# Kernel optimization log

Measured on AMD Instinct MI355X. Metric: run time of the kernel, lower is better.

The kernel has to match this reference:

```python
import jax, jax.numpy as jnp
import numpy as np

N_ITER = 10
TOL = 1e-05
EPS_R = 1e-10
REG = 1e-06
F32_EPS = float(np.finfo(np.float32).eps)


def setup_inputs() -> dict:
    key = jax.random.key(0)
    K, T, F, _ = 6, 2048, 513, 2
    X = jax.random.normal(key, (K, T, F, 2), dtype=jnp.float32)
    return {"X": X}


def _aux_iva_iss(X):
    # X: (K, T, F, 2) real/imag -> complex (F, K, T)
    Xc = (X[..., 0] + 1j * X[..., 1]).astype(jnp.complex64)
    Xc = jnp.transpose(Xc, (2, 0, 1))  # (F, K, T)
    F, K, T = Xc.shape
    eyeK = jnp.eye(K, dtype=jnp.complex64)
    W = jnp.broadcast_to(eyeK, (F, K, K)).astype(jnp.complex64)  # (F, K, K)
    Xh = jnp.conj(Xc)
    done = jnp.array(False)

    for _ in range(N_ITER):
        W_old = W
        # demix: Y[f] = W[f] @ X[f]
        Y = jnp.einsum('fkm,fmt->fkt', W, Xc)
        # per-(source, frame) norms across frequency
        r = jnp.sqrt(jnp.clip(jnp.sum(jnp.abs(Y) ** 2, axis=0), EPS_R))  # (K, T)
        wt = 1.0 / jnp.clip(r, EPS_R)  # laplace contrast g'(r)/r
        # weighted covariances V[f,k] = (X_f * wt[k]) X_f^H / T + reg*I  -> (F, K, K, K)
        V = jnp.einsum('fat,kt,fbt->fkab', Xc, wt.astype(jnp.complex64), Xh) / T
        V = V + REG * eyeK
        # sequential ISS updates over target row k (vectorized over f, m)
        for k in range(K):
            wk = W[:, k, :]  # (F, K)
            wk_c = jnp.conj(wk)
            quad = jnp.einsum('fa,fmab,fb->fm', wk, V, wk_c)  # w_k V_m w_k^H
            denom = jnp.clip(quad.real, EPS_R)  # (F, K)
            num = jnp.einsum('fma,fmab,fb->fm', W, V, wk_c)  # w_m V_m w_k^H
            vk = num / denom  # (F, K)
            vk = vk.at[:, k].set((1.0 - 1.0 / jnp.sqrt(denom[:, k])).astype(jnp.complex64))
            W = W - vk[:, :, None] * wk[:, None, :]
        # emulate early-break on relative change (freeze W once converged)
        W = jnp.where(done, W_old, W)
        diff = jnp.linalg.norm((W - W_old).reshape(-1))
        rel = diff / jnp.clip(jnp.linalg.norm(W_old.reshape(-1)), F32_EPS)
        done = jnp.logical_or(done, rel < TOL)

    Y = jnp.einsum('fkm,fmt->fkt', W, Xc)  # (F, K, T)
    # ref_mic == 0 -> no projection-back rescaling
    Y_out = jnp.transpose(Y, (1, 2, 0))  # (K, T, F)
    return jnp.stack([Y_out.real, Y_out.imag], axis=-1)  # (K, T, F, 2)


def reference(X):
    return _aux_iva_iss(X)
```

## Files before the change

### kernel.cpp

```cpp
#include <hip/hip_runtime.h>
#include <hip/hip_bf16.h>
#include <math.h>

#define T_DIM 2048
#define F_DIM 513
#define N_ITER 10

#define OFF_W    0
#define OFF_WT   36936
#define OFF_P0   49224
#define OFF_P1   50250
#define OFF_R2   51276
#define OFF_VP   51276

typedef __attribute__((ext_vector_type(8))) short bf16x8;
typedef __attribute__((ext_vector_type(4))) float f32x4;

static __device__ inline unsigned pack2bf(float a, float b) {
    union { __hip_bfloat16 h; unsigned short u; } ca, cb;
    ca.h = __float2bfloat16(a);
    cb.h = __float2bfloat16(b);
    return (unsigned)ca.u | ((unsigned)cb.u << 16);
}

__global__ __launch_bounds__(256) void transp(const float2* __restrict__ X,
                                              float2* __restrict__ Xt,
                                              float* __restrict__ ws) {
    const int fb  = blockIdx.x + 64 * (blockIdx.y + 17 * blockIdx.z);
    const int tid = threadIdx.x;
    if (fb < 73) {
        int idx = fb * 256 + tid;
        if (idx < F_DIM * 36) {
            int e = idx % 36;
            ws[OFF_W + 2 * idx]     = ((e / 6) == (e % 6)) ? 1.0f : 0.0f;
            ws[OFF_W + 2 * idx + 1] = 0.0f;
        }
    } else if (fb < 78) {
        int idx = (fb - 73) * 256 + tid;
        if (idx < 2 * F_DIM) { ws[OFF_P0 + idx] = 1.0f; ws[OFF_P1 + idx] = 1.0f; }
    }

    __shared__ float2 tile[32][33];
    const int k  = blockIdx.z;
    const int t0 = blockIdx.x * 32;
    const int f0 = blockIdx.y * 32;
    const int tx = tid & 31, ty = tid >> 5;
#pragma unroll
    for (int j = 0; j < 4; ++j) {
        int t = t0 + ty + j * 8;
        int f = f0 + tx;
        if (f < F_DIM) tile[ty + j * 8][tx] = X[((size_t)k * T_DIM + t) * F_DIM + f];
    }
    __syncthreads();
#pragma unroll
    for (int j = 0; j < 4; ++j) {
        int f = f0 + ty + j * 8;
        int t = t0 + tx;
        if (f < F_DIM) Xt[((size_t)f * 6 + k) * T_DIM + t] = tile[tx][ty + j * 8];
    }
}

__global__ __launch_bounds__(256) void passA1(const float2* __restrict__ Xt,
                                              float* __restrict__ ws,
                                              const float* __restrict__ pin) {
    __shared__ float r2s[4][6][65];
    __shared__ float sc[8];
    const int tid = threadIdx.x, wv = tid >> 6, lane = tid & 63;
    {
        float d2 = 0.f, o2 = 0.f;
        for (int i = tid; i < F_DIM; i += 256) { d2 += pin[2 * i]; o2 += pin[2 * i + 1]; }
#pragma unroll
        for (int d = 1; d < 64; d <<= 1) { d2 += __shfl_xor(d2, d); o2 += __shfl_xor(o2, d); }
        if (lane == 0) { sc[wv * 2] = d2; sc[wv * 2 + 1] = o2; }
        __syncthreads();
        d2 = sc[0] + sc[2] + sc[4] + sc[6];
        o2 = sc[1] + sc[3] + sc[5] + sc[7];
        float rel = sqrtf(d2) / fmaxf(sqrtf(o2), 1.1920929e-07f);
        if (rel < 1e-5f) return;
    }
    const int t  = blockIdx.x * 64 + lane;
    const int fc = blockIdx.y;
    const float2* Wc = (const float2*)(ws + OFF_W);
    float acc[6] = {0.f, 0.f, 0.f, 0.f, 0.f, 0.f};
#pragma unroll
    for (int i = 0; i < 4; ++i) {
        const int f = fc * 16 + wv * 4 + i;
        if (f < F_DIM) {
            const float2* xf = Xt + (size_t)f * 6 * T_DIM + t;
            float2 x[6];
#pragma unroll
            for (int m = 0; m < 6; ++m) x[m] = xf[(size_t)m * T_DIM];
            const float2* wf = Wc + f * 36;
#pragma unroll
            for (int k = 0; k < 6; ++k) {
                float yr = 0.f, yi = 0.f;
#pragma unroll
                for (int m = 0; m < 6; ++m) {
                    float2 wk = wf[k * 6 + m];
                    yr += wk.x * x[m].x - wk.y * x[m].y;
                    yi += wk.x * x[m].y + wk.y * x[m].x;
                }
                acc[k] += yr * yr + yi * yi;
            }
        }
    }
#pragma unroll
    for (int k = 0; k < 6; ++k) r2s[wv][k][lane] = acc[k];
    __syncthreads();
    for (int v = tid; v < 384; v += 256) {
        int k = v >> 6, l = v & 63;
        float s = r2s[0][k][l] + r2s[1][k][l] + r2s[2][k][l] + r2s[3][k][l];
        ws[OFF_R2 + ((size_t)fc * 6 + k) * T_DIM + blockIdx.x * 64 + l] = s;
    }
}

__global__ __launch_bounds__(256) void passA2(float* __restrict__ ws,
                                              const float* __restrict__ pin) {
    __shared__ float sc[8];
    const int tid = threadIdx.x, wv = tid >> 6, lane = tid & 63;
    {
        float d2 = 0.f, o2 = 0.f;
        for (int i = tid; i < F_DIM; i += 256) { d2 += pin[2 * i]; o2 += pin[2 * i + 1]; }
#pragma unroll
        for (int d = 1; d < 64; d <<= 1) { d2 += __shfl_xor(d2, d); o2 += __shfl_xor(o2, d); }
        if (lane == 0) { sc[wv * 2] = d2; sc[wv * 2 + 1] = o2; }
        __syncthreads();
        d2 = sc[0] + sc[2] + sc[4] + sc[6];
        o2 = sc[1] + sc[3] + sc[5] + sc[7];
        float rel = sqrtf(d2) / fmaxf(sqrtf(o2), 1.1920929e-07f);
        if (rel < 1e-5f) return;
    }
    const int idx = blockIdx.x * 256 + tid;
    float s = 0.f;
#pragma unroll
    for (int fc = 0; fc < 33; ++fc) s += ws[OFF_R2 + (size_t)fc * 6 * T_DIM + idx];
    float r = sqrtf(fmaxf(s, 1e-10f));
    ws[OFF_WT + idx] = 1.0f / fmaxf(r, 1e-10f);
}

__global__ __launch_bounds__(384) void passB(const float2* __restrict__ Xt,
                                             float* __restrict__ ws,
                                             const float* __restrict__ pin) {
    __shared__ __align__(16) char plane[16 * 528];
    __shared__ __align__(16) float gbuf[6][256];
    __shared__ float sc[12];
    const int tid = threadIdx.x, wv = tid >> 6, lane = tid & 63;

    {
        float d2 = 0.f, o2 = 0.f;
        for (int i = tid; i < F_DIM; i += 384) { d2 += pin[2 * i]; o2 += pin[2 * i + 1]; }
#pragma unroll
        for (int d = 1; d < 64; d <<= 1) { d2 += __shfl_xor(d2, d); o2 += __shfl_xor(o2, d); }
        if (lane == 0) { sc[wv * 2] = d2; sc[wv * 2 + 1] = o2; }
        __syncthreads();
        d2 = 0.f; o2 = 0.f;
#pragma unroll
        for (int w = 0; w < 6; ++w) { d2 += sc[w * 2]; o2 += sc[w * 2 + 1]; }
        float rel = sqrtf(d2) / fmaxf(sqrtf(o2), 1.1920929e-07f);
        __syncthreads();
        if (rel < 1e-5f) return;
    }

    const int f = blockIdx.x, tq = blockIdx.y;
    const float2* xb = Xt + (size_t)f * 6 * T_DIM;

    for (int i = tid; i < 528; i += 384) ((unsigned*)(plane + 12 * 528))[i] = 0;

    f32x4 acc0 = {0.f, 0.f, 0.f, 0.f};
    f32x4 acc1 = {0.f, 0.f, 0.f, 0.f};
    const int rc = lane & 15;
    const int G  = lane >> 4;
    const char* pu = plane + rc * 528 + G * 16;
    const float* gk = &gbuf[wv][0] + G * 8;

    for (int c = 0; c < 2; ++c) {
        const int t0 = tq * 512 + c * 256;
        __syncthreads();
        for (int i = tid; i < 1536; i += 384) {
            int kk = i >> 8, toff = i & 255;
            gbuf[kk][toff] = ws[OFF_WT + kk * T_DIM + t0 + toff];
        }
        for (int it = tid; it < 768; it += 384) {
            int m = it >> 7, q = it & 127;
            float4 xv = *(const float4*)(xb + (size_t)m * T_DIM + t0 + 2 * q);
            *(unsigned*)(plane + m * 528 + 4 * q)       = pack2bf(xv.x, xv.z);
            *(unsigned*)(plane + (6 + m) * 528 + 4 * q) = pack2bf(xv.y, xv.w);
        }
        __syncthreads();
#pragma unroll
        for (int s = 0; s < 8; ++s) {
            bf16x8 b = *(const bf16x8*)(pu + s * 64);
            f32x4 gA = *(const f32x4*)(gk + s * 32);
            f32x4 gB = *(const f32x4*)(gk + s * 32 + 4);
            const unsigned* bu = (const unsigned*)&b;
            bf16x8 a;
            unsigned* au = (unsigned*)&a;
            au[0] = pack2bf(__uint_as_float(bu[0] << 16) * gA[0],
                            __uint_as_float(bu[0] & 0xffff0000u) * gA[1]);
            au[1] = pack2bf(__uint_as_float(bu[1] << 16) * gA[2],
                            __uint_as_float(bu[1] & 0xffff0000u) * gA[3]);
            au[2] = pack2bf(__uint_as_float(bu[2] << 16) * gB[0],
                            __uint_as_float(bu[2] & 0xffff0000u) * gB[1]);
            au[3] = pack2bf(__uint_as_float(bu[3] << 16) * gB[2],
                            __uint_as_float(bu[3] & 0xffff0000u) * gB[3]);
            if (s & 1) acc1 = __builtin_amdgcn_mfma_f32_16x16x32_bf16(a, b, acc1, 0, 0, 0);
            else       acc0 = __builtin_amdgcn_mfma_f32_16x16x32_bf16(a, b, acc0, 0, 0, 0);
        }
    }
    __syncthreads();

    float* S = (float*)plane;
    {
        float* Sk = S + wv * 256;
#pragma unroll
        for (int r = 0; r < 4; ++r)
            Sk[(4 * G + r) * 16 + rc] = acc0[r] + acc1[r];
    }
    __syncthreads();

    if (tid < 216) {
        const int kk = tid / 36, e = tid % 36;
        const float* Sk = S + kk * 256;
        float val;
        if (e < 6) {
            val = Sk[e * 16 + e] + Sk[(6 + e) * 16 + (6 + e)];
        } else if (e < 21) {
            int p = e - 6;
            int a = (p < 1) ? 1 : (p < 3) ? 2 : (p < 6) ? 3 : (p < 10) ? 4 : 5;
            int b = p - a * (a - 1) / 2;
            val = Sk[a * 16 + b] + Sk[(6 + a) * 16 + (6 + b)];
        } else {
            int p = e - 21;
            int a = (p < 1) ? 1 : (p < 3) ? 2 : (p < 6) ? 3 : (p < 10) ? 4 : 5;
            int b = p - a * (a - 1) / 2;
            val = Sk[(6 + a) * 16 + b] - Sk[a * 16 + (6 + b)];
        }
        ws[OFF_VP + ((size_t)f * 4 + tq) * 216 + tid] = val;
    }
}

__global__ __launch_bounds__(64) void passC(float* __restrict__ ws,
                                            const float* __restrict__ pin,
                                            float* __restrict__ pout) {
    __shared__ float VL[432];
    const int f = blockIdx.x;
    const int lane = threadIdx.x;
    {
        float d2 = 0.f, o2 = 0.f;
        for (int i = lane; i < F_DIM; i += 64) { d2 += pin[2 * i]; o2 += pin[2 * i + 1]; }
#pragma unroll
        for (int d = 1; d < 64; d <<= 1) { d2 += __shfl_xor(d2, d); o2 += __shfl_xor(o2, d); }
        float rel = sqrtf(d2) / fmaxf(sqrtf(o2), 1.1920929e-07f);
        if (rel < 1e-5f) {
            if (lane == 0) { pout[2 * f] = 0.0f; pout[2 * f + 1] = 1.0f; }
            return;
        }
    }
    for (int v = lane; v < 216; v += 64) {
        float sum = 0.f;
#pragma unroll
        for (int tq = 0; tq < 4; ++tq)
            sum += ws[OFF_VP + ((size_t)f * 4 + tq) * 216 + v];
        sum *= (1.0f / (float)T_DIM);
        int kk = v / 36, e = v % 36;
        if (e < 6) {
            VL[((kk * 6 + e) * 6 + e) * 2]     = sum + 1e-6f;
            VL[((kk * 6 + e) * 6 + e) * 2 + 1] = 0.f;
        } else if (e < 21) {
            int p = e - 6;
            int a = (p < 1) ? 1 : (p < 3) ? 2 : (p < 6) ? 3 : (p < 10) ? 4 : 5;
            int b = p - a * (a - 1) / 2;
            VL[((kk * 6 + a) * 6 + b) * 2] = sum;
            VL[((kk * 6 + b) * 6 + a) * 2] = sum;
        } else {
            int p = e - 21;
            int a = (p < 1) ? 1 : (p < 3) ? 2 : (p < 6) ? 3 : (p < 10) ? 4 : 5;
            int b = p - a * (a - 1) / 2;
            VL[((kk * 6 + a) * 6 + b) * 2 + 1] =  sum;
            VL[((kk * 6 + b) * 6 + a) * 2 + 1] = -sum;
        }
    }
    __syncthreads();

    const int m = lane;
    const bool act = (m < 6);
    float w6[6][2], wold[6][2];
#pragma unroll
    for (int a = 0; a < 6; ++a) {
        w6[a][0] = 0.f; w6[a][1] = 0.f; wold[a][0] = 0.f; wold[a][1] = 0.f;
    }
    float* Wp = ws + OFF_W + ((size_t)f * 36 + (act ? m : 0) * 6) * 2;
    if (act) {
#pragma unroll
        for (int a = 0; a < 6; ++a) {
            w6[a][0] = Wp[2 * a]; w6[a][1] = Wp[2 * a + 1];
            wold[a][0] = w6[a][0]; wold[a][1] = w6[a][1];
        }
    }
    const float2* VL2 = (const float2*)VL;
    for (int kk = 0; kk < 6; ++kk) {
        float wk[6][2];
#pragma unroll
        for (int a = 0; a < 6; ++a) {
            wk[a][0] = __shfl(w6[a][0], kk);
            wk[a][1] = __shfl(w6[a][1], kk);
        }
        if (act) {
            float t6[6][2];
#pragma unroll
            for (int a = 0; a < 6; ++a) {
                float tr = 0.f, ti = 0.f;
#pragma unroll
                for (int b = 0; b < 6; ++b) {
                    float2 vv = VL2[m * 36 + a * 6 + b];
                    tr += vv.x * wk[b][0] + vv.y * wk[b][1];
                    ti += vv.y * wk[b][0] - vv.x * wk[b][1];
                }
                t6[a][0] = tr; t6[a][1] = ti;
            }
            float quad = 0.f, nr = 0.f, ni = 0.f;
#pragma unroll
            for (int a = 0; a < 6; ++a) {
                quad += wk[a][0] * t6[a][0] - wk[a][1] * t6[a][1];
                nr   += w6[a][0] * t6[a][0] - w6[a][1] * t6[a][1];
                ni   += w6[a][0] * t6[a][1] + w6[a][1] * t6[a][0];
            }
            float denom = fmaxf(quad, 1e-10f);
            float vkr, vki;
            if (m == kk) { vkr = 1.0f - 1.0f / sqrtf(denom); vki = 0.0f; }
            else { float inv = 1.0f / denom; vkr = nr * inv; vki = ni * inv; }
#pragma unroll
            for (int a = 0; a < 6; ++a) {
                w6[a][0] -= vkr * wk[a][0] - vki * wk[a][1];
                w6[a][1] -= vkr * wk[a][1] + vki * wk[a][0];
            }
        }
    }
    float d2 = 0.f, o2 = 0.f;
    if (act) {
#pragma unroll
        for (int a = 0; a < 6; ++a) {
            Wp[2 * a] = w6[a][0]; Wp[2 * a + 1] = w6[a][1];
            float dr = w6[a][0] - wold[a][0], di = w6[a][1] - wold[a][1];
            d2 += dr * dr + di * di;
            o2 += wold[a][0] * wold[a][0] + wold[a][1] * wold[a][1];
        }
    }
#pragma unroll
    for (int d = 1; d < 8; d <<= 1) {
        d2 += __shfl_xor(d2, d);
        o2 += __shfl_xor(o2, d);
    }
    if (lane == 0) {
        pout[2 * f]     = d2;
        pout[2 * f + 1] = o2;
    }
}

__global__ __launch_bounds__(256) void finalY(const float2* __restrict__ X,
                                              const float* __restrict__ ws,
                                              float2* __restrict__ out) {
    const int f  = blockIdx.y * 256 + threadIdx.x;
    const int t0 = blockIdx.x * 4;
    if (f >= F_DIM) return;
    const float2* Wf = (const float2*)(ws + OFF_W) + (size_t)f * 36;
    float2 w[36];
#pragma unroll
    for (int i = 0; i < 36; ++i) w[i] = Wf[i];
#pragma unroll
    for (int tl = 0; tl < 4; ++tl) {
        int t = t0 + tl;
        float2 x[6];
#pragma unroll
        for (int m = 0; m < 6; ++m) x[m] = X[((size_t)m * T_DIM + t) * F_DIM + f];
#pragma unroll
        for (int k = 0; k < 6; ++k) {
            float yr = 0.f, yi = 0.f;
#pragma unroll
            for (int m = 0; m < 6; ++m) {
                float2 wk = w[k * 6 + m];
                yr += wk.x * x[m].x - wk.y * x[m].y;
                yi += wk.x * x[m].y + wk.y * x[m].x;
            }
            out[((size_t)k * T_DIM + t) * F_DIM + f] = make_float2(yr, yi);
        }
    }
}

extern "C" void kernel_launch(void* const* d_in, const int* in_sizes, int n_in,
                              void* d_out, int out_size, void* d_ws, size_t ws_size,
                              hipStream_t stream) {
    (void)in_sizes; (void)n_in; (void)out_size; (void)ws_size;
    const float2* X = (const float2*)d_in[0];
    float* ws = (float*)d_ws;
    float2* out = (float2*)d_out;
    float2* Xt = out;

    transp<<<dim3(64, 17, 6), 256, 0, stream>>>(X, Xt, ws);
    for (int it = 0; it < N_ITER; ++it) {
        const float* pin = ws + (((it + 1) & 1) ? OFF_P1 : OFF_P0);
        float* pout      = ws + (((it    ) & 1) ? OFF_P1 : OFF_P0);
        passA1<<<dim3(32, 33), 256, 0, stream>>>(Xt, ws, pin);
        passA2<<<48, 256, 0, stream>>>(ws, pin);
        passB<<<dim3(F_DIM, 4), 384, 0, stream>>>(Xt, ws, pin);
        passC<<<F_DIM, 64, 0, stream>>>(ws, pin, pout);
    }
    finalY<<<dim3(T_DIM / 4, 3), 256, 0, stream>>>(X, ws, out);
}
```

Measured before the change: 620.1 us.

## Fuse ISS update into demix pass, atomically accumulate norms, fold weights into passB

Merges the previous iteration's ISS row update (old passC) into the start of the demix/norm kernel, so each block recomputes W for its 16 frequencies redundantly across time tiles. W is double-buffered to avoid read/write races. Per-frequency-chunk partial norms are combined with atomicAdd into ping-pong accumulators instead of a separate reduction kernel, and passB computes the inverse-norm weights on the fly and zeroes the next accumulator. This cuts launches per iteration from four to two, at the cost of redundant ISS compute and atomic traffic.

New measurement: 594.9 us. 4.1% less time.

```diff
diff --git a/kernel.cpp b/kernel.cpp
--- a/kernel.cpp
+++ b/kernel.cpp
@@ -6,12 +6,13 @@
 #define F_DIM 513
 #define N_ITER 10
 
-#define OFF_W    0
-#define OFF_WT   36936
-#define OFF_P0   49224
-#define OFF_P1   50250
-#define OFF_R2   51276
-#define OFF_VP   51276
+#define OFF_W0   0
+#define OFF_W1   36936
+#define OFF_P0   73872
+#define OFF_P1   74898
+#define OFF_RA0  75924
+#define OFF_RA1  88212
+#define OFF_VP   100500
 
 typedef __attribute__((ext_vector_type(8))) short bf16x8;
 typedef __attribute__((ext_vector_type(4))) float f32x4;
@@ -21,6 +22,25 @@
     ca.h = __float2bfloat16(a);
     cb.h = __float2bfloat16(b);
     return (unsigned)ca.u | ((unsigned)cb.u << 16);
+}
+
+static __device__ inline void scatterV(float* V6, int e, float sum) {
+    if (e < 6) {
+        V6[(e * 6 + e) * 2]     = sum + 1e-6f;
+        V6[(e * 6 + e) * 2 + 1] = 0.f;
+    } else if (e < 21) {
+        int p = e - 6;
+        int a = (p < 1) ? 1 : (p < 3) ? 2 : (p < 6) ? 3 : (p < 10) ? 4 : 5;
+        int b = p - a * (a - 1) / 2;
+        V6[(a * 6 + b) * 2] = sum;
+        V6[(b * 6 + a) * 2] = sum;
+    } else {
+        int p = e - 21;
+        int a = (p < 1) ? 1 : (p < 3) ? 2 : (p < 6) ? 3 : (p < 10) ? 4 : 5;
+        int b = p - a * (a - 1) / 2;
+        V6[(a * 6 + b) * 2 + 1] =  sum;
+        V6[(b * 6 + a) * 2 + 1] = -sum;
+    }
 }
 
 __global__ __launch_bounds__(256) void transp(const float2* __restrict__ X,
@@ -32,12 +52,15 @@
         int idx = fb * 256 + tid;
         if (idx < F_DIM * 36) {
             int e = idx % 36;
-            ws[OFF_W + 2 * idx]     = ((e / 6) == (e % 6)) ? 1.0f : 0.0f;
-            ws[OFF_W + 2 * idx + 1] = 0.0f;
+            ws[OFF_W0 + 2 * idx]     = ((e / 6) == (e % 6)) ? 1.0f : 0.0f;
+            ws[OFF_W0 + 2 * idx + 1] = 0.0f;
         }
     } else if (fb < 78) {
         int idx = (fb - 73) * 256 + tid;
         if (idx < 2 * F_DIM) { ws[OFF_P0 + idx] = 1.0f; ws[OFF_P1 + idx] = 1.0f; }
+    } else if (fb < 126) {
+        int idx = (fb - 78) * 256 + tid;
+        if (idx < 12288) ws[OFF_RA0 + idx] = 0.0f;
     }
 
     __shared__ float2 tile[32][33];
@@ -60,12 +83,21 @@
     }
 }
 
-__global__ __launch_bounds__(256) void passA1(const float2* __restrict__ Xt,
-                                              float* __restrict__ ws,
-                                              const float* __restrict__ pin) {
-    __shared__ float r2s[4][6][65];
+__global__ __launch_bounds__(256) void passA1C(const float2* __restrict__ Xt,
+                                               float* __restrict__ ws,
+                                               const float* __restrict__ pin,
+                                               float* __restrict__ pout,
+                                               const float* __restrict__ wOld,
+                                               float* __restrict__ wNew,
+                                               float* __restrict__ r2acc,
+                                               int do_iss) {
+    __shared__ float Wl[16][72];
+    __shared__ float VL[16][432];
     __shared__ float sc[8];
     const int tid = threadIdx.x, wv = tid >> 6, lane = tid & 63;
+    const int tc = blockIdx.x, fc = blockIdx.y;
+
+    bool frozen;
     {
         float d2 = 0.f, o2 = 0.f;
         for (int i = tid; i < F_DIM; i += 256) { d2 += pin[2 * i]; o2 += pin[2 * i + 1]; }
@@ -76,75 +108,173 @@
         d2 = sc[0] + sc[2] + sc[4] + sc[6];
         o2 = sc[1] + sc[3] + sc[5] + sc[7];
         float rel = sqrtf(d2) / fmaxf(sqrtf(o2), 1.1920929e-07f);
-        if (rel < 1e-5f) return;
-    }
-    const int t  = blockIdx.x * 64 + lane;
-    const int fc = blockIdx.y;
-    const float2* Wc = (const float2*)(ws + OFF_W);
-    float acc[6] = {0.f, 0.f, 0.f, 0.f, 0.f, 0.f};
+        frozen = (rel < 1e-5f);
+        __syncthreads();
+    }
+
+    const int fl = wv * 4 + (lane >> 4);
+    const int f  = fc * 16 + fl;
+    const int m  = lane & 15;
+    const bool act = (f < F_DIM) && (m < 6);
+
+    if (do_iss == 0) {
+        if (act) {
+            const float* Wp = wOld + ((size_t)f * 36 + m * 6) * 2;
+#pragma unroll
+            for (int a = 0; a < 6; ++a) {
+                Wl[fl][(m * 6 + a) * 2]     = Wp[2 * a];
+                Wl[fl][(m * 6 + a) * 2 + 1] = Wp[2 * a + 1];
+            }
+        }
+    } else if (frozen) {
+        if (act) {
+            const float* Wp = wOld + ((size_t)f * 36 + m * 6) * 2;
+            float* Wq = wNew + ((size_t)f * 36 + m * 6) * 2;
+#pragma unroll
+            for (int a = 0; a < 6; ++a) {
+                float v0 = Wp[2 * a], v1 = Wp[2 * a + 1];
+                Wq[2 * a] = v0; Wq[2 * a + 1] = v1;
+                Wl[fl][(m * 6 + a) * 2] = v0; Wl[fl][(m * 6 + a) * 2 + 1] = v1;
+            }
+        }
+        if (tc == 0 && m == 0 && f < F_DIM) { pout[2 * f] = 0.f; pout[2 * f + 1] = 1.f; }
+    } else {
+        if (f < F_DIM) {
+            const float* vp = ws + OFF_VP + (size_t)f * 4 * 216;
+            for (int v = m; v < 216; v += 16) {
+                float sum = (vp[v] + vp[216 + v] + vp[432 + v] + vp[648 + v]) * (1.0f / (float)T_DIM);
+                scatterV(&VL[fl][(v / 36) * 72], v % 36, sum);
+            }
+        }
+        __syncthreads();
+        float w6[6][2], wo6[6][2];
+#pragma unroll
+        for (int a = 0; a < 6; ++a) { w6[a][0] = 0.f; w6[a][1] = 0.f; wo6[a][0] = 0.f; wo6[a][1] = 0.f; }
+        if (act) {
+            const float* Wp = wOld + ((size_t)f * 36 + m * 6) * 2;
+#pragma unroll
+            for (int a = 0; a < 6; ++a) {
+                w6[a][0] = Wp[2 * a]; w6[a][1] = Wp[2 * a + 1];
+                wo6[a][0] = w6[a][0]; wo6[a][1] = w6[a][1];
+            }
+        }
+        const float2* Vm = (const float2*)&VL[fl][0];
+        for (int kk = 0; kk < 6; ++kk) {
+            float wk[6][2];
+#pragma unroll
+            for (int a = 0; a < 6; ++a) {
+                wk[a][0] = __shfl(w6[a][0], kk, 16);
+                wk[a][1] = __shfl(w6[a][1], kk, 16);
+            }
+            if (act) {
+                float t6[6][2];
+#pragma unroll
+                for (int a = 0; a < 6; ++a) {
+                    float tr = 0.f, ti = 0.f;
+#pragma unroll
+                    for (int b = 0; b < 6; ++b) {
+                        float2 vv = Vm[m * 36 + a * 6 + b];
+                        tr += vv.x * wk[b][0] + vv.y * wk[b][1];
+                        ti += vv.y * wk[b][0] - vv.x * wk[b][1];
+                    }
+                    t6[a][0] = tr; t6[a][1] = ti;
+                }
+                float quad = 0.f, nr = 0.f, ni = 0.f;
+#pragma unroll
+                for (int a = 0; a < 6; ++a) {
+                    quad += wk[a][0] * t6[a][0] - wk[a][1] * t6[a][1];
+                    nr   += w6[a][0] * t6[a][0] - w6[a][1] * t6[a][1];
+                    ni   += w6[a][0] * t6[a][1] + w6[a][1] * t6[a][0];
+                }
+                float denom = fmaxf(quad, 1e-10f);
+                float vkr, vki;
+                if (m == kk) { vkr = 1.0f - 1.0f / sqrtf(denom); vki = 0.0f; }
+                else { float inv = 1.0f / denom; vkr = nr * inv; vki = ni * inv; }
+#pragma unroll
+                for (int a = 0; a < 6; ++a) {
+                    w6[a][0] -= vkr * wk[a][0] - vki * wk[a][1];
+                    w6[a][1] -= vkr * wk[a][1] + vki * wk[a][0];
+                }
+            }
+        }
+        float d2 = 0.f, o2 = 0.f;
+        if (act) {
+            float* Wq = wNew + ((size_t)f * 36 + m * 6) * 2;
+#pragma unroll
+            for (int a = 0; a < 6; ++a) {
+                Wq[2 * a] = w6[a][0]; Wq[2 * a + 1] = w6[a][1];
+                Wl[fl][(m * 6 + a) * 2] = w6[a][0]; Wl[fl][(m * 6 + a) * 2 + 1] = w6[a][1];
+                float dr = w6[a][0] - wo6[a][0], di = w6[a][1] - wo6[a][1];
+                d2 += dr * dr + di * di;
+                o2 += wo6[a][0] * wo6[a][0] + wo6[a][1] * wo6[a][1];
+            }
+        }
+#pragma unroll
+        for (int d = 1; d < 8; d <<= 1) {
+            d2 += __shfl_xor(d2, d);
+            o2 += __shfl_xor(o2, d);
+        }
+        if (tc == 0 && m == 0 && f < F_DIM) { pout[2 * f] = d2; pout[2 * f + 1] = o2; }
+    }
+    __syncthreads();
+    if (do_iss && frozen) return;
+
+    float* r2s = &VL[0][0];
+    const int t2 = tc * 128 + lane * 2;
+    float acc[6][2];
+#pragma unroll
+    for (int k = 0; k < 6; ++k) { acc[k][0] = 0.f; acc[k][1] = 0.f; }
 #pragma unroll
     for (int i = 0; i < 4; ++i) {
-        const int f = fc * 16 + wv * 4 + i;
-        if (f < F_DIM) {
-            const float2* xf = Xt + (size_t)f * 6 * T_DIM + t;
-            float2 x[6];
-#pragma unroll
-            for (int m = 0; m < 6; ++m) x[m] = xf[(size_t)m * T_DIM];
-            const float2* wf = Wc + f * 36;
+        const int ff = fc * 16 + wv * 4 + i;
+        if (ff < F_DIM) {
+            const float2* xf = Xt + (size_t)ff * 6 * T_DIM;
+            float4 x4[6];
+#pragma unroll
+            for (int mm = 0; mm < 6; ++mm)
+                x4[mm] = *(const float4*)(xf + (size_t)mm * T_DIM + t2);
+            const float* wrow = Wl[wv * 4 + i];
 #pragma unroll
             for (int k = 0; k < 6; ++k) {
-                float yr = 0.f, yi = 0.f;
-#pragma unroll
-                for (int m = 0; m < 6; ++m) {
-                    float2 wk = wf[k * 6 + m];
-                    yr += wk.x * x[m].x - wk.y * x[m].y;
-                    yi += wk.x * x[m].y + wk.y * x[m].x;
+                float y0r = 0.f, y0i = 0.f, y1r = 0.f, y1i = 0.f;
+#pragma unroll
+                for (int mm = 0; mm < 6; ++mm) {
+                    float wr = wrow[(k * 6 + mm) * 2], wi = wrow[(k * 6 + mm) * 2 + 1];
+                    y0r += wr * x4[mm].x - wi * x4[mm].y;
+                    y0i += wr * x4[mm].y + wi * x4[mm].x;
+                    y1r += wr * x4[mm].z - wi * x4[mm].w;
+                    y1i += wr * x4[mm].w + wi * x4[mm].z;
                 }
-                acc[k] += yr * yr + yi * yi;
-            }
-        }
-    }
-#pragma unroll
-    for (int k = 0; k < 6; ++k) r2s[wv][k][lane] = acc[k];
-    __syncthreads();
-    for (int v = tid; v < 384; v += 256) {
-        int k = v >> 6, l = v & 63;
-        float s = r2s[0][k][l] + r2s[1][k][l] + r2s[2][k][l] + r2s[3][k][l];
-        ws[OFF_R2 + ((size_t)fc * 6 + k) * T_DIM + blockIdx.x * 64 + l] = s;
-    }
-}
-
-__global__ __launch_bounds__(256) void passA2(float* __restrict__ ws,
-                                              const float* __restrict__ pin) {
-    __shared__ float sc[8];
-    const int tid = threadIdx.x, wv = tid >> 6, lane = tid & 63;
-    {
-        float d2 = 0.f, o2 = 0.f;
-        for (int i = tid; i < F_DIM; i += 256) { d2 += pin[2 * i]; o2 += pin[2 * i + 1]; }
-#pragma unroll
-        for (int d = 1; d < 64; d <<= 1) { d2 += __shfl_xor(d2, d); o2 += __shfl_xor(o2, d); }
-        if (lane == 0) { sc[wv * 2] = d2; sc[wv * 2 + 1] = o2; }
-        __syncthreads();
-        d2 = sc[0] + sc[2] + sc[4] + sc[6];
-        o2 = sc[1] + sc[3] + sc[5] + sc[7];
-        float rel = sqrtf(d2) / fmaxf(sqrtf(o2), 1.1920929e-07f);
-        if (rel < 1e-5f) return;
-    }
-    const int idx = blockIdx.x * 256 + tid;
-    float s = 0.f;
-#pragma unroll
-    for (int fc = 0; fc < 33; ++fc) s += ws[OFF_R2 + (size_t)fc * 6 * T_DIM + idx];
-    float r = sqrtf(fmaxf(s, 1e-10f));
-    ws[OFF_WT + idx] = 1.0f / fmaxf(r, 1e-10f);
+                acc[k][0] += y0r * y0r + y0i * y0i;
+                acc[k][1] += y1r * y1r + y1i * y1i;
+            }
+        }
+    }
+    __syncthreads();
+#pragma unroll
+    for (int k = 0; k < 6; ++k) {
+        r2s[(wv * 6 + k) * 128 + lane * 2]     = acc[k][0];
+        r2s[(wv * 6 + k) * 128 + lane * 2 + 1] = acc[k][1];
+    }
+    __syncthreads();
+    for (int v = tid; v < 768; v += 256) {
+        int k = v >> 7, l = v & 127;
+        float s = r2s[(0 * 6 + k) * 128 + l] + r2s[(1 * 6 + k) * 128 + l]
+                + r2s[(2 * 6 + k) * 128 + l] + r2s[(3 * 6 + k) * 128 + l];
+        atomicAdd(&r2acc[k * T_DIM + tc * 128 + l], s);
+    }
 }
 
 __global__ __launch_bounds__(384) void passB(const float2* __restrict__ Xt,
                                              float* __restrict__ ws,
-                                             const float* __restrict__ pin) {
+                                             const float* __restrict__ pin,
+                                             const float* __restrict__ r2in,
+                                             float* __restrict__ r2zero) {
     __shared__ __align__(16) char plane[16 * 528];
     __shared__ __align__(16) float gbuf[6][256];
     __shared__ float sc[12];
     const int tid = threadIdx.x, wv = tid >> 6, lane = tid & 63;
+    const int f = blockIdx.x, tq = blockIdx.y;
 
     {
         float d2 = 0.f, o2 = 0.f;
@@ -161,7 +291,15 @@
         if (rel < 1e-5f) return;
     }
 
-    const int f = blockIdx.x, tq = blockIdx.y;
+    {
+        int bb = (f * 4 + tq) * 6;
+#pragma unroll
+        for (int i = 0; i < 6; ++i) {
+            int idx = bb + i;
+            if (idx < 12288) r2zero[idx] = 0.f;
+        }
+    }
+
     const float2* xb = Xt + (size_t)f * 6 * T_DIM;
 
     for (int i = tid; i < 528; i += 384) ((unsigned*)(plane + 12 * 528))[i] = 0;
@@ -178,13 +316,15 @@
         __syncthreads();
         for (int i = tid; i < 1536; i += 384) {
             int kk = i >> 8, toff = i & 255;
-            gbuf[kk][toff] = ws[OFF_WT + kk * T_DIM + t0 + toff];
+            float s = r2in[kk * T_DIM + t0 + toff];
+            float r = sqrtf(fmaxf(s, 1e-10f));
+            gbuf[kk][toff] = 1.0f / fmaxf(r, 1e-10f);
         }
         for (int it = tid; it < 768; it += 384) {
-            int m = it >> 7, q = it & 127;
-            float4 xv = *(const float4*)(xb + (size_t)m * T_DIM + t0 + 2 * q);
-            *(unsigned*)(plane + m * 528 + 4 * q)       = pack2bf(xv.x, xv.z);
-            *(unsigned*)(plane + (6 + m) * 528 + 4 * q) = pack2bf(xv.y, xv.w);
+            int mm = it >> 7, q = it & 127;
+            float4 xv = *(const float4*)(xb + (size_t)mm * T_DIM + t0 + 2 * q);
+            *(unsigned*)(plane + mm * 528 + 4 * q)       = pack2bf(xv.x, xv.z);
+            *(unsigned*)(plane + (6 + mm) * 528 + 4 * q) = pack2bf(xv.y, xv.w);
         }
         __syncthreads();
 #pragma unroll
@@ -241,7 +381,9 @@
 
 __global__ __launch_bounds__(64) void passC(float* __restrict__ ws,
                                             const float* __restrict__ pin,
-                                            float* __restrict__ pout) {
+                                            float* __restrict__ pout,
+                                            const float* __restrict__ wOld,
+                                            float* __restrict__ wNew) {
     __shared__ float VL[432];
     const int f = blockIdx.x;
     const int lane = threadIdx.x;
@@ -252,52 +394,35 @@
         for (int d = 1; d < 64; d <<= 1) { d2 += __shfl_xor(d2, d); o2 += __shfl_xor(o2, d); }
         float rel = sqrtf(d2) / fmaxf(sqrtf(o2), 1.1920929e-07f);
         if (rel < 1e-5f) {
+            for (int v = lane; v < 72; v += 64)
+                wNew[(size_t)f * 72 + v] = wOld[(size_t)f * 72 + v];
             if (lane == 0) { pout[2 * f] = 0.0f; pout[2 * f + 1] = 1.0f; }
             return;
         }
     }
-    for (int v = lane; v < 216; v += 64) {
-        float sum = 0.f;
-#pragma unroll
-        for (int tq = 0; tq < 4; ++tq)
-            sum += ws[OFF_VP + ((size_t)f * 4 + tq) * 216 + v];
-        sum *= (1.0f / (float)T_DIM);
-        int kk = v / 36, e = v % 36;
-        if (e < 6) {
-            VL[((kk * 6 + e) * 6 + e) * 2]     = sum + 1e-6f;
-            VL[((kk * 6 + e) * 6 + e) * 2 + 1] = 0.f;
-        } else if (e < 21) {
-            int p = e - 6;
-            int a = (p < 1) ? 1 : (p < 3) ? 2 : (p < 6) ? 3 : (p < 10) ? 4 : 5;
-            int b = p - a * (a - 1) / 2;
-            VL[((kk * 6 + a) * 6 + b) * 2] = sum;
-            VL[((kk * 6 + b) * 6 + a) * 2] = sum;
-        } else {
-            int p = e - 21;
-            int a = (p < 1) ? 1 : (p < 3) ? 2 : (p < 6) ? 3 : (p < 10) ? 4 : 5;
-            int b = p - a * (a - 1) / 2;
-            VL[((kk * 6 + a) * 6 + b) * 2 + 1] =  sum;
-            VL[((kk * 6 + b) * 6 + a) * 2 + 1] = -sum;
+    {
+        const float* vp = ws + OFF_VP + (size_t)f * 4 * 216;
+        for (int v = lane; v < 216; v += 64) {
+            float sum = (vp[v] + vp[216 + v] + vp[432 + v] + vp[648 + v]) * (1.0f / (float)T_DIM);
+            scatterV(&VL[(v / 36) * 72], v % 36, sum);
         }
     }
     __syncthreads();
 
     const int m = lane;
     const bool act = (m < 6);
-    float w6[6][2], wold[6][2];
-#pragma unroll
-    for (int a = 0; a < 6; ++a) {
-        w6[a][0] = 0.f; w6[a][1] = 0.f; wold[a][0] = 0.f; wold[a][1] = 0.f;
-    }
-    float* Wp = ws + OFF_W + ((size_t)f * 36 + (act ? m : 0) * 6) * 2;
+    float w6[6][2], wo6[6][2];
+#pragma unroll
+    for (int a = 0; a < 6; ++a) { w6[a][0] = 0.f; w6[a][1] = 0.f; wo6[a][0] = 0.f; wo6[a][1] = 0.f; }
     if (act) {
+        const float* Wp = wOld + ((size_t)f * 36 + m * 6) * 2;
 #pragma unroll
         for (int a = 0; a < 6; ++a) {
             w6[a][0] = Wp[2 * a]; w6[a][1] = Wp[2 * a + 1];
-            wold[a][0] = w6[a][0]; wold[a][1] = w6[a][1];
-        }
-    }
-    const float2* VL2 = (const float2*)VL;
+            wo6[a][0] = w6[a][0]; wo6[a][1] = w6[a][1];
+        }
+    }
+    const float2* Vm = (const float2*)VL;
     for (int kk = 0; kk < 6; ++kk) {
         float wk[6][2];
 #pragma unroll
@@ -312,7 +437,7 @@
                 float tr = 0.f, ti = 0.f;
 #pragma unroll
                 for (int b = 0; b < 6; ++b) {
-                    float2 vv = VL2[m * 36 + a * 6 + b];
+                    float2 vv = Vm[m * 36 + a * 6 + b];
                     tr += vv.x * wk[b][0] + vv.y * wk[b][1];
                     ti += vv.y * wk[b][0] - vv.x * wk[b][1];
                 }
@@ -338,12 +463,13 @@
     }
     float d2 = 0.f, o2 = 0.f;
     if (act) {
+        float* Wq = wNew + ((size_t)f * 36 + m * 6) * 2;
 #pragma unroll
         for (int a = 0; a < 6; ++a) {
-            Wp[2 * a] = w6[a][0]; Wp[2 * a + 1] = w6[a][1];
-            float dr = w6[a][0] - wold[a][0], di = w6[a][1] - wold[a][1];
+            Wq[2 * a] = w6[a][0]; Wq[2 * a + 1] = w6[a][1];
+            float dr = w6[a][0] - wo6[a][0], di = w6[a][1] - wo6[a][1];
             d2 += dr * dr + di * di;
-            o2 += wold[a][0] * wold[a][0] + wold[a][1] * wold[a][1];
+            o2 += wo6[a][0] * wo6[a][0] + wo6[a][1] * wo6[a][1];
         }
     }
 #pragma unroll
@@ -363,7 +489,7 @@
     const int f  = blockIdx.y * 256 + threadIdx.x;
     const int t0 = blockIdx.x * 4;
     if (f >= F_DIM) return;
-    const float2* Wf = (const float2*)(ws + OFF_W) + (size_t)f * 36;
+    const float2* Wf = (const float2*)(ws + OFF_W0) + (size_t)f * 36;
     float2 w[36];
 #pragma unroll
     for (int i = 0; i < 36; ++i) w[i] = Wf[i];
@@ -396,14 +522,19 @@
     float2* out = (float2*)d_out;
     float2* Xt = out;
 
+    float* P[2]  = {ws + OFF_P0,  ws + OFF_P1};
+    float* W[2]  = {ws + OFF_W0,  ws + OFF_W1};
+    float* RA[2] = {ws + OFF_RA0, ws + OFF_RA1};
+
     transp<<<dim3(64, 17, 6), 256, 0, stream>>>(X, Xt, ws);
     for (int it = 0; it < N_ITER; ++it) {
-        const float* pin = ws + (((it + 1) & 1) ? OFF_P1 : OFF_P0);
-        float* pout      = ws + (((it    ) & 1) ? OFF_P1 : OFF_P0);
-        passA1<<<dim3(32, 33), 256, 0, stream>>>(Xt, ws, pin);
-        passA2<<<48, 256, 0, stream>>>(ws, pin);
-        passB<<<dim3(F_DIM, 4), 384, 0, stream>>>(Xt, ws, pin);
-        passC<<<F_DIM, 64, 0, stream>>>(ws, pin, pout);
-    }
+        const float* wOld = (it == 0) ? W[0] : W[(it + 1) & 1];
+        float* wNew = W[it & 1];
+        passA1C<<<dim3(16, 33), 256, 0, stream>>>(Xt, ws, P[it & 1], P[(it + 1) & 1],
+                                                  wOld, wNew, RA[it & 1], it > 0);
+        passB<<<dim3(F_DIM, 4), 384, 0, stream>>>(Xt, ws, P[(it + 1) & 1],
+                                                  RA[it & 1], RA[(it + 1) & 1]);
+    }
+    passC<<<F_DIM, 64, 0, stream>>>(ws, P[0], P[1], W[1], W[0]);
     finalY<<<dim3(T_DIM / 4, 3), 256, 0, stream>>>(X, ws, out);
 }
```
